# Optimization experiments

Hardware: AMD Instinct MI355X
Metric: run time of the kernel (lower is better)

## Reference

```python
import jax, jax.numpy as jnp
import numpy as np

N_NODES = 100000
N_EDGES = 1600000
D_IN = 128
D_HID = 128
D_OUT = 128
N_GRAPHS = 64


def setup_inputs() -> dict:
    key = jax.random.key(0)
    ks = jax.random.split(key, 10)
    x = jax.random.normal(ks[0], (N_NODES, D_IN), dtype=jnp.float32)
    edge_index = jax.random.randint(ks[1], (2, N_EDGES), 0, N_NODES, dtype=jnp.int64)
    graph_id = jnp.sort(jax.random.randint(ks[2], (N_NODES,), 0, N_GRAPHS, dtype=jnp.int64))
    s1 = 1.0 / np.sqrt(D_IN)
    s2 = 1.0 / np.sqrt(D_HID)
    s3 = 1.0 / np.sqrt(D_OUT)
    W1 = jax.random.normal(ks[3], (D_IN, D_HID), dtype=jnp.float32) * s1
    b1 = jnp.zeros((D_HID,), dtype=jnp.float32)
    W2 = jax.random.normal(ks[4], (D_HID, D_OUT), dtype=jnp.float32) * s2
    b2 = jnp.zeros((D_OUT,), dtype=jnp.float32)
    Wr1 = jax.random.normal(ks[5], (D_OUT, D_OUT), dtype=jnp.float32) * s3
    br1 = jnp.zeros((D_OUT,), dtype=jnp.float32)
    Wr2 = jax.random.normal(ks[6], (D_OUT, D_OUT), dtype=jnp.float32) * s3
    br2 = jnp.zeros((D_OUT,), dtype=jnp.float32)
    return {"x": x, "edge_index": edge_index, "graph_id": graph_id,
            "num_graphs": N_GRAPHS, "W1": W1, "b1": b1, "W2": W2, "b2": b2,
            "Wr1": Wr1, "br1": br1, "Wr2": Wr2, "br2": br2}


def _graph_conv(h, W, b, src, dst, norm_src, norm_dst, n_nodes):
    # DGL GraphConv, norm='both': out = D_dst^{-1/2} A (D_src^{-1/2} h) W + b
    h = h * norm_src[:, None]
    h = h @ W  # project first (cheap, keeps SpMM on the smaller/equal dim)
    agg = jax.ops.segment_sum(h[src], dst, num_segments=n_nodes)
    return agg * norm_dst[:, None] + b


def reference(x, edge_index, graph_id, num_graphs, W1, b1, W2, b2, Wr1, br1, Wr2, br2):
    src, dst = edge_index[0], edge_index[1]
    n_nodes = x.shape[0]
    ones = jnp.ones((src.shape[0],), dtype=x.dtype)
    deg_out = jax.ops.segment_sum(ones, src, num_segments=n_nodes)
    deg_in = jax.ops.segment_sum(ones, dst, num_segments=n_nodes)
    norm_src = jnp.clip(deg_out, 1.0) ** -0.5
    norm_dst = jnp.clip(deg_in, 1.0) ** -0.5

    # layer 1 + relu (dropout is identity in eval mode)
    h = _graph_conv(x, W1, b1, src, dst, norm_src, norm_dst, n_nodes)
    h = jax.nn.relu(h)
    # layer 2 + relu
    h = _graph_conv(h, W2, b2, src, dst, norm_src, norm_dst, n_nodes)
    h = jax.nn.relu(h)

    # per-graph mean pooling (dgl.mean_nodes)
    sums = jax.ops.segment_sum(h, graph_id, num_segments=num_graphs)
    counts = jax.ops.segment_sum(jnp.ones((n_nodes,), dtype=h.dtype), graph_id,
                                 num_segments=num_graphs)
    hg = sums / jnp.clip(counts, 1.0)[:, None]

    # readout MLP: Linear -> ReLU -> Linear
    out = jax.nn.relu(hg @ Wr1 + br1) @ Wr2 + br2
    return (out, h)
```

## Files before the change

kernel.cpp:

```cpp
#include <hip/hip_runtime.h>
#include <math.h>


#define D 128
#define BSH 8
#define BKT 256
#define CAP 4608
#define SCHUNK 3200

typedef _Float16 half8 __attribute__((ext_vector_type(8)));
typedef _Float16 half4v __attribute__((ext_vector_type(4)));
typedef _Float16 half2v __attribute__((ext_vector_type(2)));
typedef float f32x4 __attribute__((ext_vector_type(4)));

union H8 { half8 v; half2v h[4]; };

__global__ __launch_bounds__(512) void k_build(const int* __restrict__ src,
                                               const int* __restrict__ dst,
                                               int* __restrict__ cnt_d,
                                               int* __restrict__ cnt_s,
                                               int* __restrict__ packed_d,
                                               unsigned char* __restrict__ packed_s8,
                                               const float* __restrict__ W1,
                                               const float* __restrict__ W2,
                                               _Float16* __restrict__ Wt1,
                                               _Float16* __restrict__ Wt2,
                                               const int* __restrict__ gid,
                                               int* __restrict__ gptr,
                                               int N, int E, int nbkt) {
  __shared__ int hd[512], hs[512], exd[512], exs[512], based[512], bases[512];
  __shared__ int sd[SCHUNK];
  __shared__ unsigned char ss[SCHUNK];
  const int t = threadIdx.x;
  const int bid = blockIdx.x;

  for (int idx = bid * 512 + t; idx < 2 * 128 * 128; idx += gridDim.x * 512) {
    int m = idx >> 14, i = idx & 16383;
    int k = i >> 7, n = i & 127;
    (m ? Wt2 : Wt1)[n * 128 + k] = (_Float16)((m ? W2 : W1)[i]);
  }
  if (bid == gridDim.x - 1 && t <= 64) {
    int lo = 0, hi = N;
    while (lo < hi) {
      int m = (lo + hi) >> 1;
      if (gid[m] < t) lo = m + 1; else hi = m;
    }
    gptr[t] = lo;
  }

  hd[t] = 0; hs[t] = 0;
  __syncthreads();
  const int chunk = (E + gridDim.x - 1) / gridDim.x;
  const int lo = bid * chunk, hi = min(lo + chunk, E);
  const int n = hi - lo;
  for (int i = lo + t; i < hi; i += 512) {
    atomicAdd(&hd[dst[i] >> BSH], 1);
    atomicAdd(&hs[src[i] >> BSH], 1);
  }
  __syncthreads();
  int cD = hd[t], cS = hs[t];
  for (int off = 1; off < 512; off <<= 1) {
    int ad = (t >= off) ? hd[t - off] : 0;
    int as = (t >= off) ? hs[t - off] : 0;
    __syncthreads();
    hd[t] += ad; hs[t] += as;
    __syncthreads();
  }
  exd[t] = hd[t] - cD;
  exs[t] = hs[t] - cS;
  if (t < nbkt) {
    based[t] = cD ? atomicAdd(&cnt_d[t], cD) : 0;
    bases[t] = cS ? atomicAdd(&cnt_s[t], cS) : 0;
  }
  __syncthreads();
  hd[t] = 0; hs[t] = 0;
  __syncthreads();
  for (int i = lo + t; i < hi; i += 512) {
    int s = src[i], d = dst[i];
    int b1 = d >> BSH;
    int r1 = atomicAdd(&hd[b1], 1);
    sd[exd[b1] + r1] = ((d & (BKT - 1)) << 17) | s;
    int b2 = s >> BSH;
    int r2 = atomicAdd(&hs[b2], 1);
    ss[exs[b2] + r2] = (unsigned char)(s & (BKT - 1));
  }
  __syncthreads();
  for (int i = t; i < n; i += 512) {
    int blo = 0, bhi = nbkt - 1;
    while (blo < bhi) {
      int m = (blo + bhi + 1) >> 1;
      if (exd[m] <= i) blo = m; else bhi = m - 1;
    }
    int p = based[blo] + (i - exd[blo]);
    if (p < CAP) packed_d[blo * CAP + p] = sd[i];
    blo = 0; bhi = nbkt - 1;
    while (blo < bhi) {
      int m = (blo + bhi + 1) >> 1;
      if (exs[m] <= i) blo = m; else bhi = m - 1;
    }
    p = bases[blo] + (i - exs[blo]);
    if (p < CAP) packed_s8[blo * CAP + p] = ss[i];
  }
}

__global__ __launch_bounds__(512) void k_fine(const int* __restrict__ packed_d,
                                              const int* __restrict__ cnt_d,
                                              int* __restrict__ row_lo,
                                              int* __restrict__ row_hi,
                                              int* __restrict__ csr,
                                              const unsigned char* __restrict__ packed_s8,
                                              const int* __restrict__ cnt_s,
                                              float* __restrict__ norm_src,
                                              int N, int nbkt) {
  __shared__ int hist[256];
  int t = threadIdx.x;
  if (blockIdx.x >= nbkt) {
    int b = blockIdx.x - nbkt;
    size_t lo = (size_t)b * CAP;
    int cnt = min(cnt_s[b], CAP);
    if (t < 256) hist[t] = 0;
    __syncthreads();
    for (int e = t; e < cnt; e += 512)
      atomicAdd(&hist[packed_s8[lo + e]], 1);
    __syncthreads();
    int nbase = b << BSH;
    if (t < 256 && nbase + t < N)
      norm_src[nbase + t] = rsqrtf(fmaxf((float)hist[t], 1.0f));
    return;
  }
  __shared__ int excl[256];
  __shared__ int ecache[CAP];
  __shared__ int sorted[CAP];
  int b = blockIdx.x;
  int lo = b * CAP;
  int cnt = min(cnt_d[b], CAP);
  if (t < 256) hist[t] = 0;
  __syncthreads();
  for (int e = t; e < cnt; e += 512) {
    int p = packed_d[lo + e];
    ecache[e] = p;
    atomicAdd(&hist[p >> 17], 1);
  }
  __syncthreads();
  int v = (t < 256) ? hist[t] : 0;
  for (int off = 1; off < 256; off <<= 1) {
    int a = (t >= off && t < 256) ? hist[t - off] : 0;
    __syncthreads();
    if (t < 256) hist[t] += a;
    __syncthreads();
  }
  int nbase = b << BSH;
  if (t < 256) {
    excl[t] = hist[t] - v;
    if (nbase + t < N) {
      row_lo[nbase + t] = lo + hist[t] - v;
      row_hi[nbase + t] = lo + hist[t];
    }
  }
  __syncthreads();
  if (t < 256) hist[t] = 0;
  __syncthreads();
  for (int e = t; e < cnt; e += 512) {
    int p = ecache[e];
    int dlow = p >> 17;
    int r = atomicAdd(&hist[dlow], 1);
    sorted[excl[dlow] + r] = p & 0x1FFFF;
  }
  __syncthreads();
  for (int e = t; e < cnt; e += 512)
    csr[lo + e] = sorted[e];
}

__global__ __launch_bounds__(256) void k_gemm1(const float* __restrict__ A,
                                               const _Float16* __restrict__ Wt,
                                               const float* __restrict__ scale,
                                               _Float16* __restrict__ C, int N) {
  __shared__ _Float16 As[64][136];
  __shared__ _Float16 Cs[64][128];
  const int r0 = blockIdx.x * 64;
  const int t = threadIdx.x;
  for (int i = t; i < 64 * 32; i += 256) {
    int r = i >> 5, c4 = i & 31;
    float4 v = {0.f, 0.f, 0.f, 0.f};
    if (r0 + r < N) {
      v = ((const float4*)A)[(size_t)(r0 + r) * 32 + c4];
      float s = scale[r0 + r];
      v.x *= s; v.y *= s; v.z *= s; v.w *= s;
    }
    half4v h = {(_Float16)v.x, (_Float16)v.y, (_Float16)v.z, (_Float16)v.w};
    *(half4v*)&As[r][c4 * 4] = h;
  }
  __syncthreads();
  const int w = t >> 6, l = t & 63;
  const int c = l & 15, quad = l >> 4;
  f32x4 acc[8];
#pragma unroll
  for (int nt = 0; nt < 8; ++nt) acc[nt] = (f32x4){0.f, 0.f, 0.f, 0.f};
#pragma unroll
  for (int kc = 0; kc < 4; ++kc) {
    half8 a = *(const half8*)&As[w * 16 + c][kc * 32 + quad * 8];
#pragma unroll
    for (int nt = 0; nt < 8; ++nt) {
      half8 b = *(const half8*)&Wt[(size_t)(nt * 16 + c) * 128 + kc * 32 + quad * 8];
      acc[nt] = __builtin_amdgcn_mfma_f32_16x16x32_f16(a, b, acc[nt], 0, 0, 0);
    }
  }
#pragma unroll
  for (int nt = 0; nt < 8; ++nt)
#pragma unroll
    for (int r = 0; r < 4; ++r)
      Cs[w * 16 + quad * 4 + r][nt * 16 + c] = (_Float16)acc[nt][r];
  __syncthreads();
  for (int i = t; i < 64 * 16; i += 256) {
    int r = i >> 4, c8 = i & 15;
    if (r0 + r < N)
      ((half8*)C)[(size_t)(r0 + r) * 16 + c8] = *(half8*)&Cs[r][c8 * 8];
  }
}

__global__ __launch_bounds__(256) void k_gemm2(const _Float16* __restrict__ A,
                                               const _Float16* __restrict__ Wt,
                                               _Float16* __restrict__ C, int N) {
  __shared__ _Float16 As[64][136];
  __shared__ _Float16 Cs[64][128];
  const int r0 = blockIdx.x * 64;
  const int t = threadIdx.x;
  for (int i = t; i < 64 * 16; i += 256) {
    int r = i >> 4, c8 = i & 15;
    half8 v = {0, 0, 0, 0, 0, 0, 0, 0};
    if (r0 + r < N) v = ((const half8*)A)[(size_t)(r0 + r) * 16 + c8];
    *(half8*)&As[r][c8 * 8] = v;
  }
  __syncthreads();
  const int w = t >> 6, l = t & 63;
  const int c = l & 15, quad = l >> 4;
  f32x4 acc[8];
#pragma unroll
  for (int nt = 0; nt < 8; ++nt) acc[nt] = (f32x4){0.f, 0.f, 0.f, 0.f};
#pragma unroll
  for (int kc = 0; kc < 4; ++kc) {
    half8 a = *(const half8*)&As[w * 16 + c][kc * 32 + quad * 8];
#pragma unroll
    for (int nt = 0; nt < 8; ++nt) {
      half8 b = *(const half8*)&Wt[(size_t)(nt * 16 + c) * 128 + kc * 32 + quad * 8];
      acc[nt] = __builtin_amdgcn_mfma_f32_16x16x32_f16(a, b, acc[nt], 0, 0, 0);
    }
  }
#pragma unroll
  for (int nt = 0; nt < 8; ++nt)
#pragma unroll
    for (int r = 0; r < 4; ++r)
      Cs[w * 16 + quad * 4 + r][nt * 16 + c] = (_Float16)acc[nt][r];
  __syncthreads();
  for (int i = t; i < 64 * 16; i += 256) {
    int r = i >> 4, c8 = i & 15;
    if (r0 + r < N)
      ((half8*)C)[(size_t)(r0 + r) * 16 + c8] = *(half8*)&Cs[r][c8 * 8];
  }
}

#define PK_ROW(u)                                                           \
  _Pragma("unroll")                                                         \
  for (int k = 0; k < 4; ++k) acch[k] += (u).h[k];

__device__ __forceinline__ void gather_core(const half8* __restrict__ P8,
                                            const int* __restrict__ csr,
                                            int start, int end, int cg, int eg,
                                            int lane, float* acc) {
  half2v acch[4] = {{(_Float16)0.f, (_Float16)0.f}, {(_Float16)0.f, (_Float16)0.f},
                    {(_Float16)0.f, (_Float16)0.f}, {(_Float16)0.f, (_Float16)0.f}};
  for (int s0 = start; s0 < end; s0 += 64) {
    int cnt = min(64, end - s0);
    int idx = (s0 + lane < end) ? csr[s0 + lane] : 0;
    int base = 0;
    for (; base + 16 <= cnt; base += 16) {
      int i0 = __shfl(idx, base + eg);
      int i1 = __shfl(idx, base + 4 + eg);
      int i2 = __shfl(idx, base + 8 + eg);
      int i3 = __shfl(idx, base + 12 + eg);
      H8 u0, u1, u2, u3;
      u0.v = P8[(size_t)i0 * 16 + cg];
      u1.v = P8[(size_t)i1 * 16 + cg];
      u2.v = P8[(size_t)i2 * 16 + cg];
      u3.v = P8[(size_t)i3 * 16 + cg];
      PK_ROW(u0) PK_ROW(u1) PK_ROW(u2) PK_ROW(u3)
    }
    for (; base + 4 <= cnt; base += 4) {
      int i0 = __shfl(idx, base + eg);
      H8 u0;
      u0.v = P8[(size_t)i0 * 16 + cg];
      PK_ROW(u0)
    }
    if (base < cnt) {
      int j = min(base + eg, cnt - 1);
      int i0 = __shfl(idx, j);
      if (base + eg < cnt) {
        H8 u0;
        u0.v = P8[(size_t)i0 * 16 + cg];
        PK_ROW(u0)
      }
    }
  }
#pragma unroll
  for (int k = 0; k < 4; ++k) {
    acc[2 * k]     = (float)acch[k].x;
    acc[2 * k + 1] = (float)acch[k].y;
  }
#pragma unroll
  for (int j = 0; j < 8; ++j) {
    acc[j] += __shfl_xor(acc[j], 16);
    acc[j] += __shfl_xor(acc[j], 32);
  }
}

__global__ __launch_bounds__(256) void k_gather1(const half8* __restrict__ P8,
                                                 const int* __restrict__ row_lo,
                                                 const int* __restrict__ row_hi,
                                                 const int* __restrict__ csr,
                                                 const float* __restrict__ bias,
                                                 const float* __restrict__ norm_src,
                                                 half2v* __restrict__ outH, int N) {
  int wid = (blockIdx.x * 256 + threadIdx.x) >> 6;
  if (wid >= N) return;
  int lane = threadIdx.x & 63;
  int cg = lane & 15, eg = lane >> 4;
  int start = row_lo[wid], end = row_hi[wid];
  float acc[8];
  gather_core(P8, csr, start, end, cg, eg, lane, acc);
  float nd = rsqrtf(fmaxf((float)(end - start), 1.0f));
  float ns = norm_src[wid];
  float2 b = ((const float2*)bias)[cg * 4 + eg];
  half2v o = {(_Float16)(fmaxf(acc[eg * 2] * nd + b.x, 0.f) * ns),
              (_Float16)(fmaxf(acc[eg * 2 + 1] * nd + b.y, 0.f) * ns)};
  outH[(size_t)wid * 64 + cg * 4 + eg] = o;
}

__global__ __launch_bounds__(256) void k_gather2(const half8* __restrict__ P8,
                                                 const int* __restrict__ row_lo,
                                                 const int* __restrict__ row_hi,
                                                 const int* __restrict__ csr,
                                                 const float* __restrict__ bias,
                                                 float2* __restrict__ outH, int N) {
  int wid = (blockIdx.x * 256 + threadIdx.x) >> 6;
  if (wid >= N) return;
  int lane = threadIdx.x & 63;
  int cg = lane & 15, eg = lane >> 4;
  int start = row_lo[wid], end = row_hi[wid];
  float acc[8];
  gather_core(P8, csr, start, end, cg, eg, lane, acc);
  float nd = rsqrtf(fmaxf((float)(end - start), 1.0f));
  float2 b = ((const float2*)bias)[cg * 4 + eg];
  float2 o;
  o.x = fmaxf(acc[eg * 2] * nd + b.x, 0.f);
  o.y = fmaxf(acc[eg * 2 + 1] * nd + b.y, 0.f);
  outH[(size_t)wid * 64 + cg * 4 + eg] = o;
}

__global__ __launch_bounds__(256) void k_pool(const float* __restrict__ H,
                                              const int* __restrict__ gptr,
                                              float* __restrict__ pool) {
  int g = blockIdx.x >> 3, chunk = blockIdx.x & 7;
  int col = threadIdx.x & 127, rpar = threadIdx.x >> 7;
  int s = gptr[g], e = gptr[g + 1];
  float acc = 0.0f;
  for (int r = s + chunk * 2 + rpar; r < e; r += 16)
    acc += H[(size_t)r * D + col];
  __shared__ float red[256];
  red[threadIdx.x] = acc;
  __syncthreads();
  if (rpar == 0) atomicAdd(&pool[g * D + col], acc + red[threadIdx.x + 128]);
}

__global__ __launch_bounds__(128) void k_readout(const float* __restrict__ pool,
                                                 const int* __restrict__ gptr,
                                                 const float* __restrict__ Wr1,
                                                 const float* __restrict__ br1,
                                                 const float* __restrict__ Wr2,
                                                 const float* __restrict__ br2,
                                                 float* __restrict__ out) {
  int g = blockIdx.x;
  int j = threadIdx.x;
  __shared__ float hg[D];
  __shared__ float t1[D];
  float cnt = fmaxf((float)(gptr[g + 1] - gptr[g]), 1.0f);
  hg[j] = pool[(size_t)g * D + j] / cnt;
  __syncthreads();
  float a = br1[j];
  for (int k = 0; k < D; ++k) a += hg[k] * Wr1[(size_t)k * D + j];
  t1[j] = fmaxf(a, 0.0f);
  __syncthreads();
  float b = br2[j];
  for (int k = 0; k < D; ++k) b += t1[k] * Wr2[(size_t)k * D + j];
  out[(size_t)g * D + j] = b;
}

extern "C" void kernel_launch(void* const* d_in, const int* in_sizes, int n_in,
                              void* d_out, int out_size, void* d_ws, size_t ws_size,
                              hipStream_t stream) {
  const float* x   = (const float*)d_in[0];
  const int* edge  = (const int*)d_in[1];
  const int* gid   = (const int*)d_in[2];
  const float* W1  = (const float*)d_in[4];
  const float* b1  = (const float*)d_in[5];
  const float* W2  = (const float*)d_in[6];
  const float* b2  = (const float*)d_in[7];
  const float* Wr1 = (const float*)d_in[8];
  const float* br1 = (const float*)d_in[9];
  const float* Wr2 = (const float*)d_in[10];
  const float* br2 = (const float*)d_in[11];

  const int N = in_sizes[0] / D;
  const int E = in_sizes[1] / 2;
  const int* src = edge;
  const int* dst = edge + E;
  const int nbkt = (N + BKT - 1) >> BSH;

  float* bufA     = (float*)d_ws;
  float* bufB     = bufA + (size_t)N * D;
  int* row_lo     = (int*)(bufB + (size_t)N * D);
  int* row_hi     = row_lo + N;
  int* csr        = row_hi + N;
  float* norm_src = (float*)(csr + (size_t)nbkt * CAP);
  float* pool     = norm_src + N;
  int* gptr       = (int*)(pool + 64 * D);
  int* cnt_d      = gptr + 65;
  int* cnt_s      = cnt_d + 512;
  _Float16* Wt1   = (_Float16*)(cnt_s + 512);
  _Float16* Wt2   = Wt1 + 128 * 128;
  int* packed_d   = (int*)bufA;
  unsigned char* packed_s8 = (unsigned char*)(packed_d + (size_t)nbkt * CAP);
  size_t need = ((size_t)2 * N * D + 3 * (size_t)N + (size_t)nbkt * CAP
                 + 64 * D + 65 + 1024 + 16384 + 1024) * sizeof(float);
  if (ws_size < need) return;

  float* out_g = (float*)d_out;
  float* h_out = out_g + 64 * D;

  _Float16* P   = (_Float16*)bufA;
  _Float16* h1p = (_Float16*)bufB;

  hipMemsetAsync(pool, 0, (64 * D + 65 + 1024) * sizeof(float), stream);

  const int build_grid = (E + SCHUNK - 1) / SCHUNK;
  k_build<<<build_grid, 512, 0, stream>>>(src, dst, cnt_d, cnt_s,
                                          packed_d, packed_s8,
                                          W1, W2, Wt1, Wt2, gid, gptr,
                                          N, E, nbkt);
  k_fine<<<2 * nbkt, 512, 0, stream>>>(packed_d, cnt_d, row_lo, row_hi, csr,
                                       packed_s8, cnt_s, norm_src, N, nbkt);

  const int gemm_grid = (N + 63) / 64;

  k_gemm1<<<gemm_grid, 256, 0, stream>>>(x, Wt1, norm_src, P, N);
  k_gather1<<<(N * 64 + 255) / 256, 256, 0, stream>>>(
      (const half8*)P, row_lo, row_hi, csr, b1, norm_src, (half2v*)h1p, N);

  k_gemm2<<<gemm_grid, 256, 0, stream>>>(h1p, Wt2, P, N);
  k_gather2<<<(N * 64 + 255) / 256, 256, 0, stream>>>(
      (const half8*)P, row_lo, row_hi, csr, b2, (float2*)h_out, N);

  k_pool<<<64 * 8, 256, 0, stream>>>(h_out, gptr, pool);
  k_readout<<<64, 128, 0, stream>>>(pool, gptr, Wr1, br1, Wr2, br2, out_g);
}
```

Before: 381.2 us.

## Fuse first GEMM into source-degree blocks and readout into pooling via tickets

The layer-1 projection (scale by norm_src, fp16 MFMA GEMM) now runs inside the k_fine blocks that compute source degrees, so norm_src is reused from shared memory and one kernel launch disappears. LDS is shared between the CSR-sorting path and the GEMM path through a union. The readout MLP is fused into k_pool using per-graph atomic tickets: the last block to finish a graph runs the MLP. This removes two launches, but it concentrates GEMM work on only ~391 blocks and adds fence/atomic overhead in pooling.

```diff
diff --git a/kernel.cpp b/kernel.cpp
--- a/kernel.cpp
+++ b/kernel.cpp
@@ -103,6 +103,11 @@
   }
 }
 
+union FineLds {
+  struct { int excl[256]; int ecache[CAP]; int sorted[CAP]; } d;
+  struct { _Float16 As[64][136]; _Float16 Cs[64][128]; } s;
+};
+
 __global__ __launch_bounds__(512) void k_fine(const int* __restrict__ packed_d,
                                               const int* __restrict__ cnt_d,
                                               int* __restrict__ row_lo,
@@ -111,8 +116,12 @@
                                               const unsigned char* __restrict__ packed_s8,
                                               const int* __restrict__ cnt_s,
                                               float* __restrict__ norm_src,
+                                              const float* __restrict__ x,
+                                              const _Float16* __restrict__ Wt1,
+                                              _Float16* __restrict__ P,
                                               int N, int nbkt) {
   __shared__ int hist[256];
+  __shared__ FineLds u;
   int t = threadIdx.x;
   if (blockIdx.x >= nbkt) {
     int b = blockIdx.x - nbkt;
@@ -126,11 +135,51 @@
     int nbase = b << BSH;
     if (t < 256 && nbase + t < N)
       norm_src[nbase + t] = rsqrtf(fmaxf((float)hist[t], 1.0f));
+    __syncthreads();
+    const int w = t >> 6, l = t & 63;
+    const int c = l & 15, quad = l >> 4;
+    const int strip = w & 3, chalf = w >> 2;
+    for (int ti = 0; ti < 4; ++ti) {
+      const int r0 = nbase + ti * 64;
+      for (int i = t; i < 64 * 32; i += 512) {
+        int r = i >> 5, c4 = i & 31;
+        float4 v = {0.f, 0.f, 0.f, 0.f};
+        if (r0 + r < N) {
+          v = ((const float4*)x)[(size_t)(r0 + r) * 32 + c4];
+          float s = rsqrtf(fmaxf((float)hist[ti * 64 + r], 1.0f));
+          v.x *= s; v.y *= s; v.z *= s; v.w *= s;
+        }
+        half4v h = {(_Float16)v.x, (_Float16)v.y, (_Float16)v.z, (_Float16)v.w};
+        *(half4v*)&u.s.As[r][c4 * 4] = h;
+      }
+      __syncthreads();
+      f32x4 acc[4];
+#pragma unroll
+      for (int nt = 0; nt < 4; ++nt) acc[nt] = (f32x4){0.f, 0.f, 0.f, 0.f};
+#pragma unroll
+      for (int kc = 0; kc < 4; ++kc) {
+        half8 a = *(const half8*)&u.s.As[strip * 16 + c][kc * 32 + quad * 8];
+#pragma unroll
+        for (int nt = 0; nt < 4; ++nt) {
+          half8 bb = *(const half8*)&Wt1[(size_t)(chalf * 64 + nt * 16 + c) * 128 + kc * 32 + quad * 8];
+          acc[nt] = __builtin_amdgcn_mfma_f32_16x16x32_f16(a, bb, acc[nt], 0, 0, 0);
+        }
+      }
+#pragma unroll
+      for (int nt = 0; nt < 4; ++nt)
+#pragma unroll
+        for (int r = 0; r < 4; ++r)
+          u.s.Cs[strip * 16 + quad * 4 + r][chalf * 64 + nt * 16 + c] = (_Float16)acc[nt][r];
+      __syncthreads();
+      for (int i = t; i < 64 * 16; i += 512) {
+        int r = i >> 4, c8 = i & 15;
+        if (r0 + r < N)
+          ((half8*)P)[(size_t)(r0 + r) * 16 + c8] = *(half8*)&u.s.Cs[r][c8 * 8];
+      }
+      __syncthreads();
+    }
     return;
   }
-  __shared__ int excl[256];
-  __shared__ int ecache[CAP];
-  __shared__ int sorted[CAP];
   int b = blockIdx.x;
   int lo = b * CAP;
   int cnt = min(cnt_d[b], CAP);
@@ -138,7 +187,7 @@
   __syncthreads();
   for (int e = t; e < cnt; e += 512) {
     int p = packed_d[lo + e];
-    ecache[e] = p;
+    u.d.ecache[e] = p;
     atomicAdd(&hist[p >> 17], 1);
   }
   __syncthreads();
@@ -151,7 +200,7 @@
   }
   int nbase = b << BSH;
   if (t < 256) {
-    excl[t] = hist[t] - v;
+    u.d.excl[t] = hist[t] - v;
     if (nbase + t < N) {
       row_lo[nbase + t] = lo + hist[t] - v;
       row_hi[nbase + t] = lo + hist[t];
@@ -161,61 +210,14 @@
   if (t < 256) hist[t] = 0;
   __syncthreads();
   for (int e = t; e < cnt; e += 512) {
-    int p = ecache[e];
+    int p = u.d.ecache[e];
     int dlow = p >> 17;
     int r = atomicAdd(&hist[dlow], 1);
-    sorted[excl[dlow] + r] = p & 0x1FFFF;
+    u.d.sorted[u.d.excl[dlow] + r] = p & 0x1FFFF;
   }
   __syncthreads();
   for (int e = t; e < cnt; e += 512)
-    csr[lo + e] = sorted[e];
-}
-
-__global__ __launch_bounds__(256) void k_gemm1(const float* __restrict__ A,
-                                               const _Float16* __restrict__ Wt,
-                                               const float* __restrict__ scale,
-                                               _Float16* __restrict__ C, int N) {
-  __shared__ _Float16 As[64][136];
-  __shared__ _Float16 Cs[64][128];
-  const int r0 = blockIdx.x * 64;
-  const int t = threadIdx.x;
-  for (int i = t; i < 64 * 32; i += 256) {
-    int r = i >> 5, c4 = i & 31;
-    float4 v = {0.f, 0.f, 0.f, 0.f};
-    if (r0 + r < N) {
-      v = ((const float4*)A)[(size_t)(r0 + r) * 32 + c4];
-      float s = scale[r0 + r];
-      v.x *= s; v.y *= s; v.z *= s; v.w *= s;
-    }
-    half4v h = {(_Float16)v.x, (_Float16)v.y, (_Float16)v.z, (_Float16)v.w};
-    *(half4v*)&As[r][c4 * 4] = h;
-  }
-  __syncthreads();
-  const int w = t >> 6, l = t & 63;
-  const int c = l & 15, quad = l >> 4;
-  f32x4 acc[8];
-#pragma unroll
-  for (int nt = 0; nt < 8; ++nt) acc[nt] = (f32x4){0.f, 0.f, 0.f, 0.f};
-#pragma unroll
-  for (int kc = 0; kc < 4; ++kc) {
-    half8 a = *(const half8*)&As[w * 16 + c][kc * 32 + quad * 8];
-#pragma unroll
-    for (int nt = 0; nt < 8; ++nt) {
-      half8 b = *(const half8*)&Wt[(size_t)(nt * 16 + c) * 128 + kc * 32 + quad * 8];
-      acc[nt] = __builtin_amdgcn_mfma_f32_16x16x32_f16(a, b, acc[nt], 0, 0, 0);
-    }
-  }
-#pragma unroll
-  for (int nt = 0; nt < 8; ++nt)
-#pragma unroll
-    for (int r = 0; r < 4; ++r)
-      Cs[w * 16 + quad * 4 + r][nt * 16 + c] = (_Float16)acc[nt][r];
-  __syncthreads();
-  for (int i = t; i < 64 * 16; i += 256) {
-    int r = i >> 4, c8 = i & 15;
-    if (r0 + r < N)
-      ((half8*)C)[(size_t)(r0 + r) * 16 + c8] = *(half8*)&Cs[r][c8 * 8];
-  }
+    csr[lo + e] = u.d.sorted[e];
 }
 
 __global__ __launch_bounds__(256) void k_gemm2(const _Float16* __restrict__ A,
@@ -358,40 +360,46 @@
 
 __global__ __launch_bounds__(256) void k_pool(const float* __restrict__ H,
                                               const int* __restrict__ gptr,
-                                              float* __restrict__ pool) {
+                                              float* __restrict__ pool,
+                                              int* __restrict__ tickets,
+                                              const float* __restrict__ Wr1,
+                                              const float* __restrict__ br1,
+                                              const float* __restrict__ Wr2,
+                                              const float* __restrict__ br2,
+                                              float* __restrict__ out) {
   int g = blockIdx.x >> 3, chunk = blockIdx.x & 7;
-  int col = threadIdx.x & 127, rpar = threadIdx.x >> 7;
+  int t = threadIdx.x;
+  int col = t & 127, rpar = t >> 7;
   int s = gptr[g], e = gptr[g + 1];
   float acc = 0.0f;
   for (int r = s + chunk * 2 + rpar; r < e; r += 16)
     acc += H[(size_t)r * D + col];
   __shared__ float red[256];
-  red[threadIdx.x] = acc;
-  __syncthreads();
-  if (rpar == 0) atomicAdd(&pool[g * D + col], acc + red[threadIdx.x + 128]);
-}
-
-__global__ __launch_bounds__(128) void k_readout(const float* __restrict__ pool,
-                                                 const int* __restrict__ gptr,
-                                                 const float* __restrict__ Wr1,
-                                                 const float* __restrict__ br1,
-                                                 const float* __restrict__ Wr2,
-                                                 const float* __restrict__ br2,
-                                                 float* __restrict__ out) {
-  int g = blockIdx.x;
-  int j = threadIdx.x;
+  __shared__ int ticket;
+  red[t] = acc;
+  __syncthreads();
+  if (rpar == 0) atomicAdd(&pool[g * D + col], acc + red[t + 128]);
+  __threadfence();
+  __syncthreads();
+  if (t == 0) ticket = atomicAdd(&tickets[g], 1);
+  __syncthreads();
+  if (ticket != 7) return;
   __shared__ float hg[D];
   __shared__ float t1[D];
-  float cnt = fmaxf((float)(gptr[g + 1] - gptr[g]), 1.0f);
-  hg[j] = pool[(size_t)g * D + j] / cnt;
-  __syncthreads();
-  float a = br1[j];
-  for (int k = 0; k < D; ++k) a += hg[k] * Wr1[(size_t)k * D + j];
-  t1[j] = fmaxf(a, 0.0f);
-  __syncthreads();
-  float b = br2[j];
-  for (int k = 0; k < D; ++k) b += t1[k] * Wr2[(size_t)k * D + j];
-  out[(size_t)g * D + j] = b;
+  float cntg = fmaxf((float)(e - s), 1.0f);
+  if (t < 128) hg[t] = atomicAdd(&pool[(size_t)g * D + t], 0.0f) / cntg;
+  __syncthreads();
+  if (t < 128) {
+    float a = br1[t];
+    for (int k = 0; k < D; ++k) a += hg[k] * Wr1[(size_t)k * D + t];
+    t1[t] = fmaxf(a, 0.0f);
+  }
+  __syncthreads();
+  if (t < 128) {
+    float b = br2[t];
+    for (int k = 0; k < D; ++k) b += t1[k] * Wr2[(size_t)k * D + t];
+    out[(size_t)g * D + t] = b;
+  }
 }
 
 extern "C" void kernel_launch(void* const* d_in, const int* in_sizes, int n_in,
@@ -425,12 +433,13 @@
   int* gptr       = (int*)(pool + 64 * D);
   int* cnt_d      = gptr + 65;
   int* cnt_s      = cnt_d + 512;
-  _Float16* Wt1   = (_Float16*)(cnt_s + 512);
+  int* tickets    = cnt_s + 512;
+  _Float16* Wt1   = (_Float16*)(tickets + 64);
   _Float16* Wt2   = Wt1 + 128 * 128;
   int* packed_d   = (int*)bufA;
   unsigned char* packed_s8 = (unsigned char*)(packed_d + (size_t)nbkt * CAP);
   size_t need = ((size_t)2 * N * D + 3 * (size_t)N + (size_t)nbkt * CAP
-                 + 64 * D + 65 + 1024 + 16384 + 1024) * sizeof(float);
+                 + 64 * D + 65 + 1024 + 64 + 16384 + 1024) * sizeof(float);
   if (ws_size < need) return;
 
   float* out_g = (float*)d_out;
@@ -439,7 +448,7 @@
   _Float16* P   = (_Float16*)bufA;
   _Float16* h1p = (_Float16*)bufB;
 
-  hipMemsetAsync(pool, 0, (64 * D + 65 + 1024) * sizeof(float), stream);
+  hipMemsetAsync(pool, 0, (64 * D + 65 + 1024 + 64) * sizeof(float), stream);
 
   const int build_grid = (E + SCHUNK - 1) / SCHUNK;
   k_build<<<build_grid, 512, 0, stream>>>(src, dst, cnt_d, cnt_s,
@@ -447,18 +456,17 @@
                                           W1, W2, Wt1, Wt2, gid, gptr,
                                           N, E, nbkt);
   k_fine<<<2 * nbkt, 512, 0, stream>>>(packed_d, cnt_d, row_lo, row_hi, csr,
-                                       packed_s8, cnt_s, norm_src, N, nbkt);
-
-  const int gemm_grid = (N + 63) / 64;
-
-  k_gemm1<<<gemm_grid, 256, 0, stream>>>(x, Wt1, norm_src, P, N);
+                                       packed_s8, cnt_s, norm_src,
+                                       x, Wt1, P, N, nbkt);
+
   k_gather1<<<(N * 64 + 255) / 256, 256, 0, stream>>>(
       (const half8*)P, row_lo, row_hi, csr, b1, norm_src, (half2v*)h1p, N);
 
+  const int gemm_grid = (N + 63) / 64;
   k_gemm2<<<gemm_grid, 256, 0, stream>>>(h1p, Wt2, P, N);
   k_gather2<<<(N * 64 + 255) / 256, 256, 0, stream>>>(
       (const half8*)P, row_lo, row_hi, csr, b2, (float2*)h_out, N);
 
-  k_pool<<<64 * 8, 256, 0, stream>>>(h_out, gptr, pool);
-  k_readout<<<64, 128, 0, stream>>>(pool, gptr, Wr1, br1, Wr2, br2, out_g);
-}
+  k_pool<<<64 * 8, 256, 0, stream>>>(h_out, gptr, pool, tickets,
+                                     Wr1, br1, Wr2, br2, out_g);
+}
```

Result: slower. 403.5 us (+5.9%).
